# Kernel tuning notes

Measured on AMD Instinct MI355X. Metric: run time of the kernel, lower is better.

The kernel has to match this reference:

```python
import jax, jax.numpy as jnp
import numpy as np

NTOKEN, NINP, NHID, NLAYERS = 33278, 400, 1150, 3


def _lstm_scan(x_seq, h0, c0, Wih, Whh, bih, bhh):
    # x_seq: [T,B,in], h0/c0: [B,H]; PyTorch gate order i,f,g,o
    def step(carry, x):
        h, c = carry
        gates = x @ Wih.T + bih + h @ Whh.T + bhh  # [B,4H]
        i, f, g, o = jnp.split(gates, 4, axis=-1)
        c = jax.nn.sigmoid(f) * c + jax.nn.sigmoid(i) * jnp.tanh(g)
        h = jax.nn.sigmoid(o) * jnp.tanh(c)
        return (h, c), h
    (hT, cT), hs = jax.lax.scan(step, (h0, c0), x_seq)
    return hs, hT, cT


def _causal_attention(hs):
    # hs: [T,B,H]; dot-product attention of h_t over h_{0..t} (causal)
    T = hs.shape[0]
    scores = jnp.einsum('tbh,sbh->bts', hs, hs)  # [B,T,T]
    mask = jnp.tril(jnp.ones((T, T), dtype=bool))
    scores = jnp.where(mask[None, :, :], scores, -1e30)
    attn = jax.nn.softmax(scores, axis=-1)
    return jnp.einsum('bts,sbh->tbh', attn, hs)


def setup_inputs() -> dict:
    key = jax.random.key(0)
    ks = jax.random.split(key, 24)
    T, B = 100, 64
    inp = {
        'input': jax.random.randint(ks[0], (T, B), 0, NTOKEN),
        'input2': jax.random.randint(ks[1], (T, B), 0, NTOKEN),
        'h0': jnp.zeros((1, B, NHID)), 'c0': jnp.zeros((1, B, NHID)),
        'h1': jnp.zeros((1, B, NHID)), 'c1': jnp.zeros((1, B, NHID)),
        'h2': jnp.zeros((1, B, NHID)), 'c2': jnp.zeros((1, B, NHID)),
    }
    inp['emb_W'] = jax.random.uniform(ks[2], (NTOKEN, NINP), minval=-0.1, maxval=0.1)
    in_sizes = [2 * NINP, NHID, NHID]
    for l in range(NLAYERS):
        s = 1.0 / np.sqrt(NHID)
        inp[f'W_ih{l}'] = jax.random.uniform(ks[3 + 4 * l], (4 * NHID, in_sizes[l]), minval=-s, maxval=s)
        inp[f'W_hh{l}'] = jax.random.uniform(ks[4 + 4 * l], (4 * NHID, NHID), minval=-s, maxval=s)
        inp[f'b_ih{l}'] = jax.random.uniform(ks[5 + 4 * l], (4 * NHID,), minval=-s, maxval=s)
        inp[f'b_hh{l}'] = jax.random.uniform(ks[6 + 4 * l], (4 * NHID,), minval=-s, maxval=s)
    inp['dec_W'] = jax.random.uniform(ks[20], (NTOKEN, NHID), minval=-0.1, maxval=0.1)
    inp['dec_b'] = jnp.zeros((NTOKEN,))
    return inp


def reference(input, input2, h0, c0, h1, c1, h2, c2, emb_W,
              W_ih0, W_hh0, b_ih0, b_hh0,
              W_ih1, W_hh1, b_ih1, b_hh1,
              W_ih2, W_hh2, b_ih2, b_hh2,
              dec_W, dec_b):
    # eval mode: all dropouts are identity
    emb = jnp.concatenate([emb_W[input], emb_W[input2]], axis=-1)  # [T,B,2*ninp]
    x = emb
    hcs = [(h0[0], c0[0]), (h1[0], c1[0]), (h2[0], c2[0])]
    params = [(W_ih0, W_hh0, b_ih0, b_hh0), (W_ih1, W_hh1, b_ih1, b_hh1), (W_ih2, W_hh2, b_ih2, b_hh2)]
    for l in range(NLAYERS):
        hs, hT, cT = _lstm_scan(x, hcs[l][0], hcs[l][1], *params[l])
        if l == NLAYERS - 1:
            out = _causal_attention(hs)  # attention only on last layer
        else:
            x = hs
    T, B, H = out.shape
    decoded = out.reshape(T * B, H) @ dec_W.T + dec_b  # [T*B, ntoken]
    return decoded
```

## Files before the change

### kernel.cpp

```cpp
#include <hip/hip_runtime.h>
#include <stdint.h>

typedef unsigned short ushort_t;
typedef __bf16 bf16x8 __attribute__((ext_vector_type(8)));
typedef float f32x4 __attribute__((ext_vector_type(4)));

__device__ __forceinline__ float b2f(ushort_t u) {
  union { unsigned u; float f; } v; v.u = ((unsigned)u) << 16; return v.f;
}
__device__ __forceinline__ ushort_t f2b(float f) {
  union { float f; unsigned u; } v; v.f = f;
  unsigned r = (v.u + 0x7FFFu + ((v.u >> 16) & 1u)) >> 16;
  return (ushort_t)r;
}

__device__ __forceinline__ float sigm(float x)     { return 1.f / (1.f + __expf(-x)); }
__device__ __forceinline__ float tanhfast(float x) { return 1.f - 2.f / (1.f + __expf(2.f * x)); }

__device__ __forceinline__ void store_short_wt(ushort_t* p, ushort_t v) {
  asm volatile("global_store_short %0, %1, off sc0 sc1"
               :: "v"(p), "v"((unsigned)v) : "memory");
}
__device__ __forceinline__ void store_uint_wt(unsigned* p, unsigned v) {
  asm volatile("global_store_dword %0, %1, off sc0 sc1"
               :: "v"(p), "v"(v) : "memory");
}

__device__ __forceinline__ void gload_lds16(const void* g, void* lds) {
  auto l3 = reinterpret_cast<__attribute__((address_space(3))) unsigned*>(
      reinterpret_cast<uintptr_t>(lds));
  __builtin_amdgcn_global_load_lds(reinterpret_cast<const unsigned*>(g), l3, 16, 0, 0);
}

template <bool F32OUT>
__global__ __launch_bounds__(256) void gemm_bt(
    const ushort_t* __restrict__ A, const ushort_t* __restrict__ B,
    void* __restrict__ Cv,
    const float* __restrict__ bias0, const float* __restrict__ bias1,
    int lda, int ldb, int ldc, int Kpad, int N)
{
  __shared__ alignas(16) ushort_t As[128 * 32];
  __shared__ alignas(16) ushort_t Bs[128 * 32];
  const int tid = threadIdx.x;
  const int w = tid >> 6, l = tid & 63;
  const int wr = w >> 1, wc = w & 1;

  unsigned nwg = gridDim.x * gridDim.y;
  unsigned wg = blockIdx.y * gridDim.x + blockIdx.x;
  if ((nwg & 7u) == 0u) {
    unsigned cpx = nwg >> 3;
    wg = (wg & 7u) * cpx + (wg >> 3);
  }
  const long m0 = (long)(wg % gridDim.x) * 128;
  const long n0 = (long)(wg / gridDim.x) * 128;

  const int lrow = l & 15, lk = (l >> 4) * 8;

  f32x4 acc[4][4] = {};

  const int c0 = tid, c1 = tid + 256;
  const int r0 = c0 >> 2, g0 = (c0 & 3) * 8;
  const int r1 = c1 >> 2, g1 = (c1 & 3) * 8;

  for (int k0 = 0; k0 < Kpad; k0 += 32) {
    gload_lds16(A + (m0 + r0) * lda + k0 + g0, As + c0 * 8);
    gload_lds16(A + (m0 + r1) * lda + k0 + g1, As + c1 * 8);
    gload_lds16(B + (n0 + r0) * ldb + k0 + g0, Bs + c0 * 8);
    gload_lds16(B + (n0 + r1) * ldb + k0 + g1, Bs + c1 * 8);
    __syncthreads();

    bf16x8 af[4], bfr[4];
#pragma unroll
    for (int mi = 0; mi < 4; mi++)
      af[mi] = *(const bf16x8*)(As + (wr * 64 + mi * 16 + lrow) * 32 + lk);
#pragma unroll
    for (int ni = 0; ni < 4; ni++)
      bfr[ni] = *(const bf16x8*)(Bs + (wc * 64 + ni * 16 + lrow) * 32 + lk);
#pragma unroll
    for (int mi = 0; mi < 4; mi++)
#pragma unroll
      for (int ni = 0; ni < 4; ni++)
        acc[mi][ni] = __builtin_amdgcn_mfma_f32_16x16x32_bf16(af[mi], bfr[ni], acc[mi][ni], 0, 0, 0);
    __syncthreads();
  }

  const int rbase = (l >> 4) * 4;
#pragma unroll
  for (int ni = 0; ni < 4; ni++) {
    int gcol = (int)n0 + wc * 64 + ni * 16 + lrow;
    if (gcol < N) {
      float badd = 0.f;
      if (bias0) badd += bias0[gcol];
      if (bias1) badd += bias1[gcol];
#pragma unroll
      for (int mi = 0; mi < 4; mi++) {
#pragma unroll
        for (int r = 0; r < 4; r++) {
          long grow = m0 + wr * 64 + mi * 16 + rbase + r;
          float v = acc[mi][ni][r] + badd;
          if (F32OUT) ((float*)Cv)[grow * ldc + gcol] = v;
          else        ((ushort_t*)Cv)[grow * ldc + gcol] = f2b(v);
        }
      }
    }
  }
}

__global__ __launch_bounds__(256) void lstm_layer(
    ushort_t* __restrict__ hs,
    const ushort_t* __restrict__ G,
    const ushort_t* __restrict__ Whh,
    const float* __restrict__ c_in,
    unsigned* __restrict__ flags)
{
  extern __shared__ ushort_t Bsh[];
  const int tid = threadIdx.x;
  const int w = tid >> 6, l = tid & 63;
  const int us = blockIdx.x;
  const int lrow = l & 15, hi = l >> 4, lk = hi * 8;
  const int u = us * 16 + lrow;
  const int usafe = (u < 1150) ? u : 0;
  const int row0 = w * 16 + hi * 4;
  const int x7 = lrow & 7;
  const int start = us >> 1;

  for (int ci = tid; ci < 9216; ci += 256) {
    int gate = ci / 2304;
    int rem  = ci - gate * 2304;
    int row  = rem / 144;
    int c    = rem - row * 144;
    bf16x8 v = *(const bf16x8*)(Whh + ((long)(gate * 1150 + us * 16 + row)) * 1152 + c * 8);
    *(bf16x8*)(Bsh + (((gate * 16 + row) * 144) + (c ^ (row & 7))) * 8) = v;
  }
  const ushort_t* Bg0 = Bsh + ((0 * 16 + lrow) * 144) * 8;
  const ushort_t* Bg1 = Bsh + ((1 * 16 + lrow) * 144) * 8;
  const ushort_t* Bg2 = Bsh + ((2 * 16 + lrow) * 144) * 8;
  const ushort_t* Bg3 = Bsh + ((3 * 16 + lrow) * 144) * 8;

  f32x4 cc = {};
  if (u < 1150) {
#pragma unroll
    for (int r = 0; r < 4; ++r) cc[r] = c_in[(row0 + r) * 1150 + u];
  }
  __syncthreads();

  const int s1 = l, s2 = 64 + (l & 7);

  for (int t = 0; t < 100; ++t) {
    ushort_t gvv[16];
    {
      const ushort_t* gp = G + ((long)t * 64 + row0) * 4608 + usafe;
#pragma unroll
      for (int r = 0; r < 4; ++r)
#pragma unroll
        for (int g = 0; g < 4; ++g)
          gvv[r * 4 + g] = gp[(long)r * 4608 + g * 1150];
    }

    if (t > 0) {
      if (w == 0) {
        const unsigned tt = (unsigned)t;
        unsigned f1 = (s1 == us) ? tt :
            __hip_atomic_load(flags + (s1 << 5), __ATOMIC_RELAXED, __HIP_MEMORY_SCOPE_AGENT);
        unsigned f2 = (s2 == us) ? tt :
            __hip_atomic_load(flags + (s2 << 5), __ATOMIC_RELAXED, __HIP_MEMORY_SCOPE_AGENT);
        unsigned long long p1 = __ballot(f1 >= tt);
        unsigned long long p2 = __ballot(f2 >= tt);
        while ((p1 & p2) != ~0ull) {
          __builtin_amdgcn_s_sleep(8);
          if (!((p1 >> l) & 1))
            f1 = __hip_atomic_load(flags + (s1 << 5), __ATOMIC_RELAXED, __HIP_MEMORY_SCOPE_AGENT);
          if (!((p2 >> l) & 1))
            f2 = __hip_atomic_load(flags + (s2 << 5), __ATOMIC_RELAXED, __HIP_MEMORY_SCOPE_AGENT);
          p1 = __ballot(f1 >= tt);
          p2 = __ballot(f2 >= tt);
        }
      }
      __syncthreads();
      asm volatile("" ::: "memory");
    }

    const ushort_t* hp = hs + (long)t * 73728 + (long)(w * 16 + lrow) * 1152 + lk;
    f32x4 a0 = {}, a1 = {}, a2 = {}, a3 = {};
#pragma unroll 4
    for (int i = 0; i < 36; ++i) {
      int kc = start + i; if (kc >= 36) kc -= 36;
      bf16x8 a = *(const bf16x8*)(hp + kc * 32);
      int pc8 = ((kc * 4 + hi) ^ x7) * 8;
      a0 = __builtin_amdgcn_mfma_f32_16x16x32_bf16(a, *(const bf16x8*)(Bg0 + pc8), a0, 0, 0, 0);
      a1 = __builtin_amdgcn_mfma_f32_16x16x32_bf16(a, *(const bf16x8*)(Bg1 + pc8), a1, 0, 0, 0);
      a2 = __builtin_amdgcn_mfma_f32_16x16x32_bf16(a, *(const bf16x8*)(Bg2 + pc8), a2, 0, 0, 0);
      a3 = __builtin_amdgcn_mfma_f32_16x16x32_bf16(a, *(const bf16x8*)(Bg3 + pc8), a3, 0, 0, 0);
    }

    if (u < 1150) {
#pragma unroll
      for (int r = 0; r < 4; ++r) {
        float iv = a0[r] + b2f(gvv[r * 4 + 0]);
        float fv = a1[r] + b2f(gvv[r * 4 + 1]);
        float gg = a2[r] + b2f(gvv[r * 4 + 2]);
        float ov = a3[r] + b2f(gvv[r * 4 + 3]);
        float cn = sigm(fv) * cc[r] + sigm(iv) * tanhfast(gg);
        cc[r] = cn;
        float hv = sigm(ov) * tanhfast(cn);
        store_short_wt(hs + (long)(t + 1) * 73728 + (long)(row0 + r) * 1152 + u, f2b(hv));
      }
    }

    if (t != 99) {
      asm volatile("s_waitcnt vmcnt(0)" ::: "memory");
      __syncthreads();
      if (tid == 0) store_uint_wt(flags + (us << 5), (unsigned)(t + 1));
    }
  }
}

__global__ __launch_bounds__(256) void attn_kernel(
    const ushort_t* __restrict__ hs2,
    ushort_t* __restrict__ outp)
{
  __shared__ float qf[1152];
  __shared__ float sc[104];
  __shared__ float sinv;
  const int rowi = blockIdx.x;
  const int t = rowi >> 6, b = rowi & 63;
  const int tid = threadIdx.x;
  const int w = tid >> 6, l = tid & 63;

  const ushort_t* q = hs2 + (long)rowi * 1152;
  for (int c = tid; c < 1150; c += 256) qf[c] = b2f(q[c]);
  __syncthreads();

  for (int s = w; s <= t; s += 4) {
    const ushort_t* k = hs2 + (long)(s * 64 + b) * 1152;
    float p = 0.f;
    for (int h = l; h < 1150; h += 64) p += qf[h] * b2f(k[h]);
    for (int off = 32; off; off >>= 1) p += __shfl_down(p, off);
    if (l == 0) sc[s] = p;
  }
  __syncthreads();

  if (w == 0) {
    float m = -1e30f;
    for (int s = l; s <= t; s += 64) m = fmaxf(m, sc[s]);
    for (int off = 32; off; off >>= 1) m = fmaxf(m, __shfl_down(m, off));
    m = __shfl(m, 0);
    float sum = 0.f;
    for (int s = l; s <= t; s += 64) { float e = __expf(sc[s] - m); sc[s] = e; sum += e; }
    for (int off = 32; off; off >>= 1) sum += __shfl_down(sum, off);
    if (l == 0) sinv = 1.f / sum;
  }
  __syncthreads();

  const float si = sinv;
  for (int h = tid; h < 1150; h += 256) {
    float a = 0.f;
    for (int s = 0; s <= t; s++) a += sc[s] * b2f(hs2[(long)(s * 64 + b) * 1152 + h]);
    outp[(long)rowi * 1152 + h] = f2b(a * si);
  }
  if (tid < 2) outp[(long)rowi * 1152 + 1150 + tid] = 0;
}

__global__ void embed_kernel(const int* __restrict__ in1, const int* __restrict__ in2,
                             const float* __restrict__ emb, ushort_t* __restrict__ x0)
{
  int rowi = blockIdx.x;
  int l = threadIdx.x;
  long r1 = (long)in1[rowi] * 400, r2 = (long)in2[rowi] * 400;
  ushort_t* d = x0 + (long)rowi * 800;
  for (int c = l; c < 800; c += 64)
    d[c] = f2b(c < 400 ? emb[r1 + c] : emb[r2 + c - 400]);
}

__global__ void pad_convert(const float* __restrict__ in, ushort_t* __restrict__ out,
                            int R, int Cin, int total, int Cp)
{
  int idx = blockIdx.x * 256 + threadIdx.x;
  if (idx >= total) return;
  int r = idx / Cp, c = idx - r * Cp;
  float v = (r < R && c < Cin) ? in[(long)r * Cin + c] : 0.f;
  out[idx] = f2b(v);
}

__global__ void init_state(const float* __restrict__ h_in,
                           ushort_t* __restrict__ hs, unsigned* __restrict__ flags)
{
  int idx = blockIdx.x * 256 + threadIdx.x;
  if (idx < 72 * 32) flags[idx] = 0u;
  if (idx < 64 * 1152) {
    int b = idx / 1152, c = idx - b * 1152;
    hs[idx] = (c < 1150) ? f2b(h_in[b * 1150 + c]) : (ushort_t)0;
  }
  if (idx < 100 * 128) {
    int t = idx >> 7, r = idx & 127, b = r >> 1, k = r & 1;
    hs[(long)(t + 1) * 73728 + b * 1152 + 1150 + k] = 0;
  }
}

extern "C" void kernel_launch(void* const* d_in, const int* in_sizes, int n_in,
                              void* d_out, int out_size, void* d_ws, size_t ws_size,
                              hipStream_t stream) {
  (void)in_sizes; (void)n_in; (void)out_size; (void)ws_size;
  const int* input  = (const int*)d_in[0];
  const int* input2 = (const int*)d_in[1];
  const float* h_in[3] = {(const float*)d_in[2], (const float*)d_in[4], (const float*)d_in[6]};
  const float* c_in[3] = {(const float*)d_in[3], (const float*)d_in[5], (const float*)d_in[7]};
  const float* emb_W = (const float*)d_in[8];
  const float* W_ih[3] = {(const float*)d_in[9],  (const float*)d_in[13], (const float*)d_in[17]};
  const float* W_hh[3] = {(const float*)d_in[10], (const float*)d_in[14], (const float*)d_in[18]};
  const float* b_ih[3] = {(const float*)d_in[11], (const float*)d_in[15], (const float*)d_in[19]};
  const float* b_hh[3] = {(const float*)d_in[12], (const float*)d_in[16], (const float*)d_in[20]};
  const float* dec_W = (const float*)d_in[21];
  const float* dec_b = (const float*)d_in[22];
  float* out = (float*)d_out;

  hipFuncSetAttribute((const void*)lstm_layer,
                      hipFuncAttributeMaxDynamicSharedMemorySize, 147456);

  char* base = (char*)d_ws;
  size_t off = 0;
  auto walloc = [&](size_t bytes) { char* r = base + off; off += (bytes + 255) & ~(size_t)255; return r; };
  ushort_t* decWp = (ushort_t*)walloc(33280ull * 1152 * 2);
  ushort_t* attnB = (ushort_t*)walloc(6400ull * 1152 * 2);
  unsigned* flags = (unsigned*)walloc(72 * 128 + 256);

  char* ob = (char*)d_out;
  ushort_t* G   = (ushort_t*)(ob + 0);
  ushort_t* x0  = (ushort_t*)(ob + 58982400);
  ushort_t* Wp  = (ushort_t*)(ob + 69222400);
  ushort_t* Whp = (ushort_t*)(ob + 79839232);
  ushort_t* hsA = (ushort_t*)(ob + 90456064);
  ushort_t* hsB = (ushort_t*)(ob + 105349120);

  embed_kernel<<<6400, 64, 0, stream>>>(input, input2, emb_W, x0);

  ushort_t* hcur[3] = {hsA, hsB, hsA};
  const ushort_t* X = x0;
  int lda = 800, Kp = 800;
  for (int lyr = 0; lyr < 3; lyr++) {
    if (lyr == 0) {
      int tot = 4608 * 800;
      pad_convert<<<(tot + 255) / 256, 256, 0, stream>>>(W_ih[0], Wp, 4600, 800, tot, 800);
    } else {
      int tot = 4608 * 1152;
      pad_convert<<<(tot + 255) / 256, 256, 0, stream>>>(W_ih[lyr], Wp, 4600, 1150, tot, 1152);
    }
    {
      int tot = 4608 * 1152;
      pad_convert<<<(tot + 255) / 256, 256, 0, stream>>>(W_hh[lyr], Whp, 4600, 1150, tot, 1152);
    }
    gemm_bt<false><<<dim3(50, 36), 256, 0, stream>>>(X, Wp, (void*)G, b_ih[lyr], b_hh[lyr],
                                                     lda, Kp, 4608, Kp, 4600);
    init_state<<<288, 256, 0, stream>>>(h_in[lyr], hcur[lyr], flags);
    lstm_layer<<<72, 256, 147456, stream>>>(hcur[lyr], G, Whp, c_in[lyr], flags);
    X = hcur[lyr] + 73728;
    lda = 1152; Kp = 1152;
  }

  attn_kernel<<<6400, 256, 0, stream>>>(hsA + 73728, attnB);

  {
    int tot = 33280 * 1152;
    pad_convert<<<(tot + 255) / 256, 256, 0, stream>>>(dec_W, decWp, 33278, 1150, tot, 1152);
  }

  gemm_bt<true><<<dim3(50, 260), 256, 0, stream>>>(attnB, decWp, (void*)out, dec_b, nullptr,
                                                   1152, 1152, 33278, 1152, 33278);
}
```

Before: 3.997 ms.

## Enlarge GEMM tiles to 256x256 with 512 threads and vectorized transposed-output stores

```diff
diff --git a/kernel.cpp b/kernel.cpp
--- a/kernel.cpp
+++ b/kernel.cpp
@@ -4,6 +4,7 @@
 typedef unsigned short ushort_t;
 typedef __bf16 bf16x8 __attribute__((ext_vector_type(8)));
 typedef float f32x4 __attribute__((ext_vector_type(4)));
+typedef float f32x2 __attribute__((ext_vector_type(2)));
 
 __device__ __forceinline__ float b2f(ushort_t u) {
   union { unsigned u; float f; } v; v.u = ((unsigned)u) << 16; return v.f;
@@ -33,32 +34,33 @@
 }
 
 template <bool F32OUT>
-__global__ __launch_bounds__(256) void gemm_bt(
+__global__ __launch_bounds__(512) void gemm_bt(
     const ushort_t* __restrict__ A, const ushort_t* __restrict__ B,
     void* __restrict__ Cv,
     const float* __restrict__ bias0, const float* __restrict__ bias1,
-    int lda, int ldb, int ldc, int Kpad, int N)
-{
-  __shared__ alignas(16) ushort_t As[128 * 32];
-  __shared__ alignas(16) ushort_t Bs[128 * 32];
+    int lda, int ldb, long ldc, int Kpad, int N)
+{
+  __shared__ alignas(16) ushort_t As[256 * 32];
+  __shared__ alignas(16) ushort_t Bs[256 * 32];
   const int tid = threadIdx.x;
   const int w = tid >> 6, l = tid & 63;
-  const int wr = w >> 1, wc = w & 1;
+  const int wr = w >> 2, wc = w & 3;
 
   unsigned nwg = gridDim.x * gridDim.y;
   unsigned wg = blockIdx.y * gridDim.x + blockIdx.x;
-  if ((nwg & 7u) == 0u) {
-    unsigned cpx = nwg >> 3;
-    wg = (wg & 7u) * cpx + (wg >> 3);
-  }
-  const long m0 = (long)(wg % gridDim.x) * 128;
-  const long n0 = (long)(wg / gridDim.x) * 128;
-
-  const int lrow = l & 15, lk = (l >> 4) * 8;
-
-  f32x4 acc[4][4] = {};
-
-  const int c0 = tid, c1 = tid + 256;
+  {
+    unsigned q = nwg >> 3, r = nwg & 7u;
+    unsigned xcd = wg & 7u, idx = wg >> 3;
+    wg = (xcd < r ? xcd * (q + 1) : r * (q + 1) + (xcd - r) * q) + idx;
+  }
+  const long m0 = (long)(wg % gridDim.x) * 256;
+  const long n0 = (long)(wg / gridDim.x) * 256;
+
+  const int lrow = l & 15, hi = l >> 4, lk = hi * 8;
+
+  f32x4 acc[8][4] = {};
+
+  const int c0 = tid, c1 = tid + 512;
   const int r0 = c0 >> 2, g0 = (c0 & 3) * 8;
   const int r1 = c1 >> 2, g1 = (c1 & 3) * 8;
 
@@ -69,37 +71,50 @@
     gload_lds16(B + (n0 + r1) * ldb + k0 + g1, Bs + c1 * 8);
     __syncthreads();
 
-    bf16x8 af[4], bfr[4];
-#pragma unroll
-    for (int mi = 0; mi < 4; mi++)
-      af[mi] = *(const bf16x8*)(As + (wr * 64 + mi * 16 + lrow) * 32 + lk);
+    bf16x8 af[8], bfr[4];
+#pragma unroll
+    for (int mi = 0; mi < 8; mi++)
+      af[mi] = *(const bf16x8*)(As + (wr * 128 + mi * 16 + lrow) * 32 + lk);
 #pragma unroll
     for (int ni = 0; ni < 4; ni++)
       bfr[ni] = *(const bf16x8*)(Bs + (wc * 64 + ni * 16 + lrow) * 32 + lk);
 #pragma unroll
-    for (int mi = 0; mi < 4; mi++)
+    for (int mi = 0; mi < 8; mi++)
 #pragma unroll
       for (int ni = 0; ni < 4; ni++)
-        acc[mi][ni] = __builtin_amdgcn_mfma_f32_16x16x32_bf16(af[mi], bfr[ni], acc[mi][ni], 0, 0, 0);
+        acc[mi][ni] = __builtin_amdgcn_mfma_f32_16x16x32_bf16(bfr[ni], af[mi], acc[mi][ni], 0, 0, 0);
     __syncthreads();
   }
 
-  const int rbase = (l >> 4) * 4;
 #pragma unroll
   for (int ni = 0; ni < 4; ni++) {
-    int gcol = (int)n0 + wc * 64 + ni * 16 + lrow;
-    if (gcol < N) {
-      float badd = 0.f;
-      if (bias0) badd += bias0[gcol];
-      if (bias1) badd += bias1[gcol];
-#pragma unroll
-      for (int mi = 0; mi < 4; mi++) {
-#pragma unroll
-        for (int r = 0; r < 4; r++) {
-          long grow = m0 + wr * 64 + mi * 16 + rbase + r;
-          float v = acc[mi][ni][r] + badd;
-          if (F32OUT) ((float*)Cv)[grow * ldc + gcol] = v;
-          else        ((ushort_t*)Cv)[grow * ldc + gcol] = f2b(v);
+    int gc = (int)n0 + wc * 64 + ni * 16 + hi * 4;
+    float b4[4];
+#pragma unroll
+    for (int r = 0; r < 4; r++) {
+      float bb = 0.f;
+      if (gc + r < N) {
+        if (bias0) bb += bias0[gc + r];
+        if (bias1) bb += bias1[gc + r];
+      }
+      b4[r] = bb;
+    }
+#pragma unroll
+    for (int mi = 0; mi < 8; mi++) {
+      long grow = m0 + wr * 128 + mi * 16 + lrow;
+      if (F32OUT) {
+        float* crow = (float*)Cv + grow * ldc;
+        f32x2 v01 = {acc[mi][ni][0] + b4[0], acc[mi][ni][1] + b4[1]};
+        f32x2 v23 = {acc[mi][ni][2] + b4[2], acc[mi][ni][3] + b4[3]};
+        if (gc < N)     __builtin_nontemporal_store(v01, (f32x2*)(crow + gc));
+        if (gc + 2 < N) __builtin_nontemporal_store(v23, (f32x2*)(crow + gc + 2));
+      } else {
+        if (gc < N) {
+          ushort_t* crow = (ushort_t*)Cv + grow * ldc;
+          union { ushort_t s[4]; unsigned long long u; } pk;
+#pragma unroll
+          for (int r = 0; r < 4; r++) pk.s[r] = f2b(acc[mi][ni][r] + b4[r]);
+          *(unsigned long long*)(crow + gc) = pk.u;
         }
       }
     }
@@ -349,8 +364,8 @@
       int tot = 4608 * 1152;
       pad_convert<<<(tot + 255) / 256, 256, 0, stream>>>(W_hh[lyr], Whp, 4600, 1150, tot, 1152);
     }
-    gemm_bt<false><<<dim3(50, 36), 256, 0, stream>>>(X, Wp, (void*)G, b_ih[lyr], b_hh[lyr],
-                                                     lda, Kp, 4608, Kp, 4600);
+    gemm_bt<false><<<dim3(25, 18), 512, 0, stream>>>(X, Wp, (void*)G, b_ih[lyr], b_hh[lyr],
+                                                     lda, Kp, 4608L, Kp, 4600);
     init_state<<<288, 256, 0, stream>>>(h_in[lyr], hcur[lyr], flags);
     lstm_layer<<<72, 256, 147456, stream>>>(hcur[lyr], G, Whp, c_in[lyr], flags);
     X = hcur[lyr] + 73728;
@@ -364,6 +379,6 @@
     pad_convert<<<(tot + 255) / 256, 256, 0, stream>>>(dec_W, decWp, 33278, 1150, tot, 1152);
   }
 
-  gemm_bt<true><<<dim3(50, 260), 256, 0, stream>>>(attnB, decWp, (void*)out, dec_b, nullptr,
-                                                   1152, 1152, 33278, 1152, 33278);
-}
+  gemm_bt<true><<<dim3(25, 130), 512, 0, stream>>>(attnB, decWp, (void*)out, dec_b, nullptr,
+                                                   1152, 1152, 33278L, 1152, 33278);
+}
```

Result: slower. 5.043 ms (+26.2%).
